# Kernel optimization log

Hardware: AMD Instinct MI355X
Metric: run time of the kernel (lower is better)

## Reference

```python
import jax, jax.numpy as jnp
import numpy as np

N_NODES = 100000
N_EDGES = 3200000
IN_CH = 128
HID = 64
OUT_CH = 2
BN_EPS = 1e-5


def setup_inputs() -> dict:
    key = jax.random.key(0)
    ks = jax.random.split(key, 16)
    def glorot(k, shape):
        fan_in, fan_out = shape[0], shape[1]
        lim = jnp.sqrt(6.0 / (fan_in + fan_out))
        return jax.random.uniform(k, shape, jnp.float32, -lim, lim)
    inp = {
        "x": jax.random.normal(ks[0], (N_NODES, IN_CH), jnp.float32),
        "edge_index": jax.random.randint(ks[1], (2, N_EDGES), 0, N_NODES, jnp.int64),
        # input projection + input BN
        "Wp": glorot(ks[2], (IN_CH, HID)),
        "bp": jnp.zeros((HID,), jnp.float32),
        "g_in": jnp.ones((HID,), jnp.float32),
        "b_in": jnp.zeros((HID,), jnp.float32),
        # SAGEConv layer 0: lin_l (aggr, with bias) + lin_r (self, no bias)
        "Wl0": glorot(ks[3], (HID, HID)),
        "bl0": jnp.zeros((HID,), jnp.float32),
        "Wr0": glorot(ks[4], (HID, HID)),
        "g0": jnp.ones((HID,), jnp.float32),
        "b0": jnp.zeros((HID,), jnp.float32),
        # SAGEConv layer 1
        "Wl1": glorot(ks[5], (HID, HID)),
        "bl1": jnp.zeros((HID,), jnp.float32),
        "Wr1": glorot(ks[6], (HID, HID)),
        "g1": jnp.ones((HID,), jnp.float32),
        "b1": jnp.zeros((HID,), jnp.float32),
        # output head
        "Wo": glorot(ks[7], (HID, OUT_CH)),
        "bo": jnp.zeros((OUT_CH,), jnp.float32),
    }
    return inp


def _bn(h, g, b):
    # training-mode batchnorm over node dim (biased variance, as torch)
    m = h.mean(axis=0)
    v = h.var(axis=0)
    return g * (h - m) * jax.lax.rsqrt(v + BN_EPS) + b


def _sage_conv(h, src, dst, Wl, bl, Wr):
    # mean aggregation of source features at destination nodes
    msg = h[src]                                              # [E, HID]
    summed = jax.ops.segment_sum(msg, dst, num_segments=N_NODES)
    cnt = jax.ops.segment_sum(jnp.ones((src.shape[0],), h.dtype), dst,
                              num_segments=N_NODES)
    aggr = summed / jnp.maximum(cnt, 1.0)[:, None]
    return aggr @ Wl + bl + h @ Wr


def reference(x, edge_index, Wp, bp, g_in, b_in,
              Wl0, bl0, Wr0, g0, b0,
              Wl1, bl1, Wr1, g1, b1,
              Wo, bo):
    src, dst = edge_index[0], edge_index[1]
    h = jax.nn.relu(_bn(x @ Wp + bp, g_in, b_in))   # dropout: eval no-op
    h_prev = h
    # layer 0 (i=0: no residual)
    h_new = jax.nn.relu(_bn(_sage_conv(h, src, dst, Wl0, bl0, Wr0), g0, b0))
    h_prev, h = h, h_new
    # layer 1 (i=1: residual with h_prev)
    h_new = jax.nn.relu(_bn(_sage_conv(h, src, dst, Wl1, bl1, Wr1), g1, b1))
    h_new = h_new + h_prev
    h = h_new
    return h @ Wo + bo
```

## Files before the change

### kernel.cpp

```cpp
#include <hip/hip_runtime.h>
#include <hip/hip_bf16.h>

#define NN 100000
#define NE 3200000
#define IC 128
#define HD 64
#define BN_EPS 1e-5f
#define NBUK 196
#define MSB 16

__device__ __forceinline__ float bf2f(unsigned short u) {
  return __uint_as_float(((unsigned)u) << 16);
}
__device__ __forceinline__ unsigned int f2bf(float f) {
  unsigned int u = __float_as_uint(f);
  return (u + 0x7FFFu + ((u >> 16) & 1u)) >> 16;
}
__device__ __forceinline__ unsigned int pack2(float a, float b) {
  return f2bf(a) | (f2bf(b) << 16);
}

__global__ __launch_bounds__(256) void k_gemm_in(
    const float* __restrict__ x, const float* __restrict__ Wp,
    const float* __restrict__ bp, unsigned int* __restrict__ pre16,
    float* __restrict__ stats) {
  __shared__ float sW[IC * HD];
  __shared__ unsigned int sXu[64 * 68];
  __shared__ float sStS[256], sStQ[256];
  int tid = threadIdx.x;
  for (int i = tid; i < IC * HD / 4; i += 256)
    *(float4*)&sW[i * 4] = *(const float4*)&Wp[i * 4];
  int cg = tid & 15, rg = tid >> 4;
  int c0 = cg * 4;
  float4 bpc = *(const float4*)&bp[c0];
  float S[4] = {0.f, 0.f, 0.f, 0.f}, Q[4] = {0.f, 0.f, 0.f, 0.f};
  const int NT = (NN + 63) / 64;
  for (int t = blockIdx.x; t < NT; t += gridDim.x) {
    int row0 = t * 64;
    __syncthreads();
    for (int i = tid; i < 1024; i += 256) {
      int r = i >> 4, k8 = i & 15;
      int grow = row0 + r;
      if (grow >= NN) grow = NN - 1;
      const float* xs = &x[(size_t)grow * IC + k8 * 8];
      float4 f0 = *(const float4*)xs;
      float4 f1 = *(const float4*)(xs + 4);
      uint4 p;
      p.x = pack2(f0.x, f0.y);
      p.y = pack2(f0.z, f0.w);
      p.z = pack2(f1.x, f1.y);
      p.w = pack2(f1.z, f1.w);
      *(uint4*)&sXu[r * 68 + k8 * 4] = p;
    }
    __syncthreads();
    float acc[4][4];
#pragma unroll
    for (int r = 0; r < 4; ++r)
#pragma unroll
      for (int c = 0; c < 4; ++c) acc[r][c] = ((const float*)&bpc)[c];
    for (int kg = 0; kg < IC; kg += 4) {
      uint2 xu[4];
      float4 wv[4];
#pragma unroll
      for (int r = 0; r < 4; ++r)
        xu[r] = *(const uint2*)&sXu[(rg * 4 + r) * 68 + (kg >> 1)];
#pragma unroll
      for (int j = 0; j < 4; ++j)
        wv[j] = *(const float4*)&sW[(kg + j) * HD + c0];
#pragma unroll
      for (int r = 0; r < 4; ++r) {
        float xv[4];
        xv[0] = __uint_as_float(xu[r].x << 16);
        xv[1] = __uint_as_float(xu[r].x & 0xFFFF0000u);
        xv[2] = __uint_as_float(xu[r].y << 16);
        xv[3] = __uint_as_float(xu[r].y & 0xFFFF0000u);
#pragma unroll
        for (int j = 0; j < 4; ++j) {
#pragma unroll
          for (int c = 0; c < 4; ++c)
            acc[r][c] = fmaf(xv[j], ((const float*)&wv[j])[c], acc[r][c]);
        }
      }
    }
#pragma unroll
    for (int r = 0; r < 4; ++r) {
      int row = row0 + rg * 4 + r;
      if (row < NN) {
        uint2 o;
        o.x = pack2(acc[r][0], acc[r][1]);
        o.y = pack2(acc[r][2], acc[r][3]);
        *(uint2*)&pre16[(size_t)row * 32 + cg * 2] = o;
#pragma unroll
        for (int c = 0; c < 4; ++c) {
          S[c] += acc[r][c];
          Q[c] = fmaf(acc[r][c], acc[r][c], Q[c]);
        }
      }
    }
  }
#pragma unroll
  for (int c = 0; c < 4; ++c) {
    S[c] += __shfl_xor(S[c], 16);
    S[c] += __shfl_xor(S[c], 32);
    Q[c] += __shfl_xor(Q[c], 16);
    Q[c] += __shfl_xor(Q[c], 32);
  }
  int wave = tid >> 6, lane = tid & 63;
  if (lane < 16) {
#pragma unroll
    for (int c = 0; c < 4; ++c) {
      sStS[wave * 64 + lane * 4 + c] = S[c];
      sStQ[wave * 64 + lane * 4 + c] = Q[c];
    }
  }
  __syncthreads();
  if (tid < 64) {
    float Ts = sStS[tid] + sStS[64 + tid] + sStS[128 + tid] + sStS[192 + tid];
    float Tq = sStQ[tid] + sStQ[64 + tid] + sStQ[128 + tid] + sStQ[192 + tid];
    atomicAdd(&stats[tid], Ts);
    atomicAdd(&stats[64 + tid], Tq);
  }
}

__global__ __launch_bounds__(256) void k_bn_relu(
    const unsigned int* __restrict__ pre16, const float* __restrict__ stats,
    const float* __restrict__ g, const float* __restrict__ b,
    unsigned int* __restrict__ h16u) {
  size_t i = (size_t)blockIdx.x * 256 + threadIdx.x;
  int c0 = ((int)(i & 15)) * 4;
  const float invN = 1.0f / NN;
  uint2 p = *(const uint2*)&pre16[i * 2];
  float v[4];
  v[0] = __uint_as_float(p.x << 16);
  v[1] = __uint_as_float(p.x & 0xFFFF0000u);
  v[2] = __uint_as_float(p.y << 16);
  v[3] = __uint_as_float(p.y & 0xFFFF0000u);
#pragma unroll
  for (int c = 0; c < 4; ++c) {
    float m = stats[c0 + c] * invN;
    float var = stats[64 + c0 + c] * invN - m * m;
    float sc = g[c0 + c] * rsqrtf(var + BN_EPS);
    v[c] = fmaxf((v[c] - m) * sc + b[c0 + c], 0.f);
  }
  uint2 o;
  o.x = pack2(v[0], v[1]);
  o.y = pack2(v[2], v[3]);
  *(uint2*)&h16u[i * 2] = o;
}

__global__ __launch_bounds__(256) void k_bhist(
    const int* __restrict__ dst, unsigned int* __restrict__ bcnt) {
  __shared__ unsigned int h[NBUK];
  for (int i = threadIdx.x; i < NBUK; i += 256) h[i] = 0u;
  __syncthreads();
  int i0 = blockIdx.x * 256 + threadIdx.x;
  int stride = gridDim.x * 256;
  for (int e = i0; e < NE; e += stride)
    atomicAdd(&h[((unsigned)dst[e]) >> 9], 1u);
  __syncthreads();
  for (int i = threadIdx.x; i < NBUK; i += 256)
    if (h[i]) atomicAdd(&bcnt[i], h[i]);
}

__global__ __launch_bounds__(256) void k_bscan(
    const unsigned int* __restrict__ bcnt, unsigned int* __restrict__ gstart,
    unsigned int* __restrict__ gcur) {
  __shared__ unsigned int s[256];
  int t = threadIdx.x;
  unsigned int my = (t < NBUK) ? bcnt[t] : 0u;
  s[t] = my;
  __syncthreads();
  for (int off = 1; off < 256; off <<= 1) {
    unsigned int v = (t >= off) ? s[t - off] : 0u;
    __syncthreads();
    s[t] += v;
    __syncthreads();
  }
  if (t < NBUK) {
    gstart[t] = s[t] - my;
    gcur[t] = s[t] - my;
  }
  if (t == NBUK - 1) gstart[NBUK] = s[t];
}

__global__ __launch_bounds__(256) void k_msplit(
    const int* __restrict__ src, const int* __restrict__ dst,
    unsigned int* __restrict__ gcur, unsigned int* __restrict__ staging) {
  __shared__ unsigned int hist[NBUK];
  __shared__ unsigned int gbase[NBUK];
  int tid = threadIdx.x;
  for (int i = tid; i < NBUK; i += 256) hist[i] = 0u;
  __syncthreads();
  int e0 = blockIdx.x * (256 * MSB);
  unsigned int pk[MSB], rk[MSB], bk[MSB];
#pragma unroll
  for (int i = 0; i < MSB; ++i) {
    int e = e0 + i * 256 + tid;
    if (e < NE) {
      int d = dst[e];
      unsigned int b = (unsigned int)(d >> 9);
      rk[i] = atomicAdd(&hist[b], 1u);
      pk[i] = (unsigned int)src[e] | ((unsigned int)(d & 511) << 17);
      bk[i] = b;
    } else {
      bk[i] = 0xFFFFFFFFu;
    }
  }
  __syncthreads();
  for (int i = tid; i < NBUK; i += 256)
    if (hist[i]) gbase[i] = atomicAdd(&gcur[i], hist[i]);
  __syncthreads();
#pragma unroll
  for (int i = 0; i < MSB; ++i)
    if (bk[i] != 0xFFFFFFFFu) staging[gbase[bk[i]] + rk[i]] = pk[i];
}

__global__ __launch_bounds__(512) void k_bucket_sort(
    const unsigned int* __restrict__ staging,
    const unsigned int* __restrict__ gstart, unsigned int* __restrict__ nstart,
    unsigned int* __restrict__ srcoff) {
  __shared__ unsigned int hist[512];
  __shared__ unsigned int sc[512];
  __shared__ unsigned int cur[512];
  int b = blockIdx.x, t = threadIdx.x;
  hist[t] = 0u;
  __syncthreads();
  int lo = (int)gstart[b], hi = (int)gstart[b + 1];
  for (int e = lo + t; e < hi; e += 512)
    atomicAdd(&hist[staging[e] >> 17], 1u);
  __syncthreads();
  unsigned int my = hist[t];
  sc[t] = my;
  __syncthreads();
  for (int off = 1; off < 512; off <<= 1) {
    unsigned int v = (t >= off) ? sc[t - off] : 0u;
    __syncthreads();
    sc[t] += v;
    __syncthreads();
  }
  unsigned int st = (unsigned int)lo + sc[t] - my;
  cur[t] = st;
  int node = b * 512 + t;
  if (node < NN) {
    nstart[node] = st;
    if (node == NN - 1) nstart[NN] = st + my;
  }
  __syncthreads();
  for (int e = lo + t; e < hi; e += 512) {
    unsigned int u = staging[e];
    unsigned int pos = atomicAdd(&cur[u >> 17], 1u);
    srcoff[pos] = (u & 0x1FFFFu) << 7;
  }
}

__global__ __launch_bounds__(256) void k_aggr_sorted(
    const unsigned int* __restrict__ srcoff,
    const unsigned int* __restrict__ nstart,
    const unsigned short* __restrict__ h16,
    unsigned short* __restrict__ a16) {
  int lane = threadIdx.x & 63;
  int n = (int)((blockIdx.x * 256 + threadIdx.x) >> 6);
  if (n >= NN) return;
  int g = lane >> 3;
  int q = lane & 7;
  int e0 = (int)nstart[n];
  int e1 = (int)nstart[n + 1];
  const char* hbase = (const char*)h16 + q * 16;
  float a0 = 0.f, a1 = 0.f, a2 = 0.f, a3 = 0.f;
  float a4 = 0.f, a5 = 0.f, a6 = 0.f, a7 = 0.f;
  float b0 = 0.f, b1 = 0.f, b2 = 0.f, b3 = 0.f;
  float b4 = 0.f, b5 = 0.f, b6 = 0.f, b7 = 0.f;
  int e = e0 + g;
  for (; e + 8 < e1; e += 16) {
    unsigned int o0 = srcoff[e];
    unsigned int o1 = srcoff[e + 8];
    uint4 u0 = *(const uint4*)(hbase + o0);
    uint4 u1 = *(const uint4*)(hbase + o1);
    a0 += __uint_as_float(u0.x << 16);
    a1 += __uint_as_float(u0.x & 0xFFFF0000u);
    a2 += __uint_as_float(u0.y << 16);
    a3 += __uint_as_float(u0.y & 0xFFFF0000u);
    a4 += __uint_as_float(u0.z << 16);
    a5 += __uint_as_float(u0.z & 0xFFFF0000u);
    a6 += __uint_as_float(u0.w << 16);
    a7 += __uint_as_float(u0.w & 0xFFFF0000u);
    b0 += __uint_as_float(u1.x << 16);
    b1 += __uint_as_float(u1.x & 0xFFFF0000u);
    b2 += __uint_as_float(u1.y << 16);
    b3 += __uint_as_float(u1.y & 0xFFFF0000u);
    b4 += __uint_as_float(u1.z << 16);
    b5 += __uint_as_float(u1.z & 0xFFFF0000u);
    b6 += __uint_as_float(u1.w << 16);
    b7 += __uint_as_float(u1.w & 0xFFFF0000u);
  }
  if (e < e1) {
    unsigned int o0 = srcoff[e];
    uint4 u0 = *(const uint4*)(hbase + o0);
    a0 += __uint_as_float(u0.x << 16);
    a1 += __uint_as_float(u0.x & 0xFFFF0000u);
    a2 += __uint_as_float(u0.y << 16);
    a3 += __uint_as_float(u0.y & 0xFFFF0000u);
    a4 += __uint_as_float(u0.z << 16);
    a5 += __uint_as_float(u0.z & 0xFFFF0000u);
    a6 += __uint_as_float(u0.w << 16);
    a7 += __uint_as_float(u0.w & 0xFFFF0000u);
  }
  a0 += b0; a1 += b1; a2 += b2; a3 += b3;
  a4 += b4; a5 += b5; a6 += b6; a7 += b7;
#pragma unroll
  for (int off = 8; off <= 32; off <<= 1) {
    a0 += __shfl_xor(a0, off);
    a1 += __shfl_xor(a1, off);
    a2 += __shfl_xor(a2, off);
    a3 += __shfl_xor(a3, off);
    a4 += __shfl_xor(a4, off);
    a5 += __shfl_xor(a5, off);
    a6 += __shfl_xor(a6, off);
    a7 += __shfl_xor(a7, off);
  }
  if (g == 0) {
    float cntf = (float)(e1 - e0);
    float inv = (cntf > 0.f) ? 1.0f / cntf : 0.f;
    uint4 o;
    o.x = pack2(a0 * inv, a1 * inv);
    o.y = pack2(a2 * inv, a3 * inv);
    o.z = pack2(a4 * inv, a5 * inv);
    o.w = pack2(a6 * inv, a7 * inv);
    *(uint4*)((char*)a16 + (size_t)n * 128 + q * 16) = o;
  }
}

__global__ __launch_bounds__(256) void k_combine(
    const unsigned int* __restrict__ a16u,
    const unsigned int* __restrict__ h16u, const float* __restrict__ Wl,
    const float* __restrict__ bl, const float* __restrict__ Wr,
    unsigned int* __restrict__ pre16, float* __restrict__ stats) {
  __shared__ float sWl[HD * HD], sWr[HD * HD];
  __shared__ unsigned int sAu[64 * 36], sHu[64 * 36];
  __shared__ float sStS[256], sStQ[256];
  int tid = threadIdx.x;
  for (int i = tid; i < HD * HD / 4; i += 256) {
    *(float4*)&sWl[i * 4] = *(const float4*)&Wl[i * 4];
    *(float4*)&sWr[i * 4] = *(const float4*)&Wr[i * 4];
  }
  int cg = tid & 15, rg = tid >> 4;
  int c0 = cg * 4;
  float4 blc = *(const float4*)&bl[c0];
  float S[4] = {0.f, 0.f, 0.f, 0.f}, Q[4] = {0.f, 0.f, 0.f, 0.f};
  const int NT = (NN + 63) / 64;
  for (int t = blockIdx.x; t < NT; t += gridDim.x) {
    int row0 = t * 64;
    __syncthreads();
    for (int i = tid; i < 512; i += 256) {
      int r = i >> 3, c4 = i & 7;
      int grow = row0 + r;
      if (grow >= NN) grow = NN - 1;
      *(uint4*)&sAu[r * 36 + c4 * 4] =
          *(const uint4*)&a16u[(size_t)grow * 32 + c4 * 4];
      *(uint4*)&sHu[r * 36 + c4 * 4] =
          *(const uint4*)&h16u[(size_t)grow * 32 + c4 * 4];
    }
    __syncthreads();
    float acc[4][4];
#pragma unroll
    for (int r = 0; r < 4; ++r)
#pragma unroll
      for (int c = 0; c < 4; ++c) acc[r][c] = ((const float*)&blc)[c];
    for (int kg = 0; kg < HD; kg += 4) {
      uint2 au[4], hu[4];
      float4 wlv[4], wrv[4];
#pragma unroll
      for (int r = 0; r < 4; ++r) {
        au[r] = *(const uint2*)&sAu[(rg * 4 + r) * 36 + (kg >> 1)];
        hu[r] = *(const uint2*)&sHu[(rg * 4 + r) * 36 + (kg >> 1)];
      }
#pragma unroll
      for (int j = 0; j < 4; ++j) {
        wlv[j] = *(const float4*)&sWl[(kg + j) * HD + c0];
        wrv[j] = *(const float4*)&sWr[(kg + j) * HD + c0];
      }
#pragma unroll
      for (int r = 0; r < 4; ++r) {
        float av[4], hv[4];
        av[0] = __uint_as_float(au[r].x << 16);
        av[1] = __uint_as_float(au[r].x & 0xFFFF0000u);
        av[2] = __uint_as_float(au[r].y << 16);
        av[3] = __uint_as_float(au[r].y & 0xFFFF0000u);
        hv[0] = __uint_as_float(hu[r].x << 16);
        hv[1] = __uint_as_float(hu[r].x & 0xFFFF0000u);
        hv[2] = __uint_as_float(hu[r].y << 16);
        hv[3] = __uint_as_float(hu[r].y & 0xFFFF0000u);
#pragma unroll
        for (int j = 0; j < 4; ++j) {
#pragma unroll
          for (int c = 0; c < 4; ++c) {
            acc[r][c] = fmaf(av[j], ((const float*)&wlv[j])[c], acc[r][c]);
            acc[r][c] = fmaf(hv[j], ((const float*)&wrv[j])[c], acc[r][c]);
          }
        }
      }
    }
#pragma unroll
    for (int r = 0; r < 4; ++r) {
      int row = row0 + rg * 4 + r;
      if (row < NN) {
        uint2 o;
        o.x = pack2(acc[r][0], acc[r][1]);
        o.y = pack2(acc[r][2], acc[r][3]);
        *(uint2*)&pre16[(size_t)row * 32 + cg * 2] = o;
#pragma unroll
        for (int c = 0; c < 4; ++c) {
          S[c] += acc[r][c];
          Q[c] = fmaf(acc[r][c], acc[r][c], Q[c]);
        }
      }
    }
  }
#pragma unroll
  for (int c = 0; c < 4; ++c) {
    S[c] += __shfl_xor(S[c], 16);
    S[c] += __shfl_xor(S[c], 32);
    Q[c] += __shfl_xor(Q[c], 16);
    Q[c] += __shfl_xor(Q[c], 32);
  }
  int wave = tid >> 6, lane = tid & 63;
  if (lane < 16) {
#pragma unroll
    for (int c = 0; c < 4; ++c) {
      sStS[wave * 64 + lane * 4 + c] = S[c];
      sStQ[wave * 64 + lane * 4 + c] = Q[c];
    }
  }
  __syncthreads();
  if (tid < 64) {
    float Ts = sStS[tid] + sStS[64 + tid] + sStS[128 + tid] + sStS[192 + tid];
    float Tq = sStQ[tid] + sStQ[64 + tid] + sStQ[128 + tid] + sStQ[192 + tid];
    atomicAdd(&stats[tid], Ts);
    atomicAdd(&stats[64 + tid], Tq);
  }
}

__global__ __launch_bounds__(256) void k_bn_relu_head(
    const unsigned short* __restrict__ pre16,
    const float* __restrict__ stats, const float* __restrict__ g,
    const float* __restrict__ b, const unsigned short* __restrict__ resid16,
    const float* __restrict__ Wo, const float* __restrict__ bo,
    float* __restrict__ out) {
  int lane = threadIdx.x & 63;
  int wid = (int)((blockIdx.x * blockDim.x + threadIdx.x) >> 6);
  int nw = (int)((gridDim.x * blockDim.x) >> 6);
  const float invN = 1.0f / NN;
  float m = stats[lane] * invN;
  float v = stats[64 + lane] * invN - m * m;
  float sc = g[lane] * rsqrtf(v + BN_EPS);
  float bb = b[lane];
  float w0 = Wo[lane * 2], w1 = Wo[lane * 2 + 1];
  float b0 = bo[0], b1 = bo[1];
  for (int row = wid; row < NN; row += nw) {
    size_t i = (size_t)row * HD + lane;
    float val = (bf2f(pre16[i]) - m) * sc + bb;
    val = fmaxf(val, 0.f) + bf2f(resid16[i]);
    float a0 = val * w0, a1 = val * w1;
#pragma unroll
    for (int off = 32; off > 0; off >>= 1) {
      a0 += __shfl_down(a0, off);
      a1 += __shfl_down(a1, off);
    }
    if (lane == 0) {
      out[(size_t)row * 2] = a0 + b0;
      out[(size_t)row * 2 + 1] = a1 + b1;
    }
  }
}

extern "C" void kernel_launch(void* const* d_in, const int* in_sizes, int n_in,
                              void* d_out, int out_size, void* d_ws,
                              size_t ws_size, hipStream_t stream) {
  const float* x = (const float*)d_in[0];
  const int* ei = (const int*)d_in[1];
  const float* Wp = (const float*)d_in[2];
  const float* bp = (const float*)d_in[3];
  const float* g_in = (const float*)d_in[4];
  const float* b_in = (const float*)d_in[5];
  const float* Wl0 = (const float*)d_in[6];
  const float* bl0 = (const float*)d_in[7];
  const float* Wr0 = (const float*)d_in[8];
  const float* g0 = (const float*)d_in[9];
  const float* b0 = (const float*)d_in[10];
  const float* Wl1 = (const float*)d_in[11];
  const float* bl1 = (const float*)d_in[12];
  const float* Wr1 = (const float*)d_in[13];
  const float* g1 = (const float*)d_in[14];
  const float* b1 = (const float*)d_in[15];
  const float* Wo = (const float*)d_in[16];
  const float* bo = (const float*)d_in[17];
  float* out = (float*)d_out;

  const int* src = ei;
  const int* dst = ei + NE;

  unsigned int* pre16 = (unsigned int*)d_ws;
  unsigned short* h0 = (unsigned short*)(pre16 + (size_t)NN * 32);
  unsigned short* h1 = h0 + (size_t)NN * HD;
  unsigned short* a16 = h1 + (size_t)NN * HD;
  unsigned int* staging = (unsigned int*)(a16 + (size_t)NN * HD);
  unsigned int* srcoff = staging + NE;
  unsigned int* nstart = srcoff + NE;
  unsigned int* bcnt = nstart + NN + 1;
  unsigned int* gstart = bcnt + NBUK;
  unsigned int* gcur = gstart + NBUK + 1;
  float* stats0 = (float*)(gcur + NBUK);
  float* stats1 = stats0 + 128;
  float* stats2 = stats1 + 128;

  const int BNR_BLOCKS = (NN * HD / 4) / 256;
  const int AGGR_BLOCKS = 25000;
  const int MS_BLOCKS = (NE + 256 * MSB - 1) / (256 * MSB);

  hipMemsetAsync(stats0, 0, 3 * 128 * sizeof(float), stream);
  hipMemsetAsync(bcnt, 0, NBUK * sizeof(unsigned int), stream);

  k_gemm_in<<<768, 256, 0, stream>>>(x, Wp, bp, pre16, stats0);
  k_bn_relu<<<BNR_BLOCKS, 256, 0, stream>>>(pre16, stats0, g_in, b_in,
                                            (unsigned int*)h0);

  k_bhist<<<1024, 256, 0, stream>>>(dst, bcnt);
  k_bscan<<<1, 256, 0, stream>>>(bcnt, gstart, gcur);
  k_msplit<<<MS_BLOCKS, 256, 0, stream>>>(src, dst, gcur, staging);
  k_bucket_sort<<<NBUK, 512, 0, stream>>>(staging, gstart, nstart, srcoff);

  k_aggr_sorted<<<AGGR_BLOCKS, 256, 0, stream>>>(srcoff, nstart, h0, a16);
  k_combine<<<768, 256, 0, stream>>>((const unsigned int*)a16,
                                     (const unsigned int*)h0, Wl0, bl0, Wr0,
                                     pre16, stats1);
  k_bn_relu<<<BNR_BLOCKS, 256, 0, stream>>>(pre16, stats1, g0, b0,
                                            (unsigned int*)h1);

  k_aggr_sorted<<<AGGR_BLOCKS, 256, 0, stream>>>(srcoff, nstart, h1, a16);
  k_combine<<<768, 256, 0, stream>>>((const unsigned int*)a16,
                                     (const unsigned int*)h1, Wl1, bl1, Wr1,
                                     pre16, stats2);
  k_bn_relu_head<<<1024, 256, 0, stream>>>((const unsigned short*)pre16,
                                           stats2, g1, b1, h0, Wo, bo, out);
}
```

Baseline: 395.8 us.

## Drop dst histogram pass via fixed-capacity buckets; one tile per GEMM block

```diff
diff --git a/kernel.cpp b/kernel.cpp
--- a/kernel.cpp
+++ b/kernel.cpp
@@ -8,6 +8,7 @@
 #define BN_EPS 1e-5f
 #define NBUK 196
 #define MSB 16
+#define CAP 20480
 
 __device__ __forceinline__ float bf2f(unsigned short u) {
   return __uint_as_float(((unsigned)u) << 16);
@@ -24,77 +25,70 @@
     const float* __restrict__ x, const float* __restrict__ Wp,
     const float* __restrict__ bp, unsigned int* __restrict__ pre16,
     float* __restrict__ stats) {
-  __shared__ float sW[IC * HD];
   __shared__ unsigned int sXu[64 * 68];
   __shared__ float sStS[256], sStQ[256];
   int tid = threadIdx.x;
-  for (int i = tid; i < IC * HD / 4; i += 256)
-    *(float4*)&sW[i * 4] = *(const float4*)&Wp[i * 4];
   int cg = tid & 15, rg = tid >> 4;
   int c0 = cg * 4;
+  int row0 = blockIdx.x * 64;
+  for (int i = tid; i < 1024; i += 256) {
+    int r = i >> 4, k8 = i & 15;
+    int grow = row0 + r;
+    if (grow >= NN) grow = NN - 1;
+    const float* xs = &x[(size_t)grow * IC + k8 * 8];
+    float4 f0 = *(const float4*)xs;
+    float4 f1 = *(const float4*)(xs + 4);
+    uint4 p;
+    p.x = pack2(f0.x, f0.y);
+    p.y = pack2(f0.z, f0.w);
+    p.z = pack2(f1.x, f1.y);
+    p.w = pack2(f1.z, f1.w);
+    *(uint4*)&sXu[r * 68 + k8 * 4] = p;
+  }
+  __syncthreads();
   float4 bpc = *(const float4*)&bp[c0];
+  float acc[4][4];
+#pragma unroll
+  for (int r = 0; r < 4; ++r)
+#pragma unroll
+    for (int c = 0; c < 4; ++c) acc[r][c] = ((const float*)&bpc)[c];
+  for (int kg = 0; kg < IC; kg += 4) {
+    uint2 xu[4];
+    float4 wv[4];
+#pragma unroll
+    for (int r = 0; r < 4; ++r)
+      xu[r] = *(const uint2*)&sXu[(rg * 4 + r) * 68 + (kg >> 1)];
+#pragma unroll
+    for (int j = 0; j < 4; ++j)
+      wv[j] = *(const float4*)&Wp[(size_t)(kg + j) * HD + c0];
+#pragma unroll
+    for (int r = 0; r < 4; ++r) {
+      float xv[4];
+      xv[0] = __uint_as_float(xu[r].x << 16);
+      xv[1] = __uint_as_float(xu[r].x & 0xFFFF0000u);
+      xv[2] = __uint_as_float(xu[r].y << 16);
+      xv[3] = __uint_as_float(xu[r].y & 0xFFFF0000u);
+#pragma unroll
+      for (int j = 0; j < 4; ++j) {
+#pragma unroll
+        for (int c = 0; c < 4; ++c)
+          acc[r][c] = fmaf(xv[j], ((const float*)&wv[j])[c], acc[r][c]);
+      }
+    }
+  }
   float S[4] = {0.f, 0.f, 0.f, 0.f}, Q[4] = {0.f, 0.f, 0.f, 0.f};
-  const int NT = (NN + 63) / 64;
-  for (int t = blockIdx.x; t < NT; t += gridDim.x) {
-    int row0 = t * 64;
-    __syncthreads();
-    for (int i = tid; i < 1024; i += 256) {
-      int r = i >> 4, k8 = i & 15;
-      int grow = row0 + r;
-      if (grow >= NN) grow = NN - 1;
-      const float* xs = &x[(size_t)grow * IC + k8 * 8];
-      float4 f0 = *(const float4*)xs;
-      float4 f1 = *(const float4*)(xs + 4);
-      uint4 p;
-      p.x = pack2(f0.x, f0.y);
-      p.y = pack2(f0.z, f0.w);
-      p.z = pack2(f1.x, f1.y);
-      p.w = pack2(f1.z, f1.w);
-      *(uint4*)&sXu[r * 68 + k8 * 4] = p;
-    }
-    __syncthreads();
-    float acc[4][4];
-#pragma unroll
-    for (int r = 0; r < 4; ++r)
-#pragma unroll
-      for (int c = 0; c < 4; ++c) acc[r][c] = ((const float*)&bpc)[c];
-    for (int kg = 0; kg < IC; kg += 4) {
-      uint2 xu[4];
-      float4 wv[4];
-#pragma unroll
-      for (int r = 0; r < 4; ++r)
-        xu[r] = *(const uint2*)&sXu[(rg * 4 + r) * 68 + (kg >> 1)];
-#pragma unroll
-      for (int j = 0; j < 4; ++j)
-        wv[j] = *(const float4*)&sW[(kg + j) * HD + c0];
-#pragma unroll
-      for (int r = 0; r < 4; ++r) {
-        float xv[4];
-        xv[0] = __uint_as_float(xu[r].x << 16);
-        xv[1] = __uint_as_float(xu[r].x & 0xFFFF0000u);
-        xv[2] = __uint_as_float(xu[r].y << 16);
-        xv[3] = __uint_as_float(xu[r].y & 0xFFFF0000u);
-#pragma unroll
-        for (int j = 0; j < 4; ++j) {
-#pragma unroll
-          for (int c = 0; c < 4; ++c)
-            acc[r][c] = fmaf(xv[j], ((const float*)&wv[j])[c], acc[r][c]);
-        }
-      }
-    }
-#pragma unroll
-    for (int r = 0; r < 4; ++r) {
-      int row = row0 + rg * 4 + r;
-      if (row < NN) {
-        uint2 o;
-        o.x = pack2(acc[r][0], acc[r][1]);
-        o.y = pack2(acc[r][2], acc[r][3]);
-        *(uint2*)&pre16[(size_t)row * 32 + cg * 2] = o;
-#pragma unroll
-        for (int c = 0; c < 4; ++c) {
-          S[c] += acc[r][c];
-          Q[c] = fmaf(acc[r][c], acc[r][c], Q[c]);
-        }
+#pragma unroll
+  for (int r = 0; r < 4; ++r) {
+    int row = row0 + rg * 4 + r;
+    if (row < NN) {
+      uint2 o;
+      o.x = pack2(acc[r][0], acc[r][1]);
+      o.y = pack2(acc[r][2], acc[r][3]);
+      *(uint2*)&pre16[(size_t)row * 32 + cg * 2] = o;
+#pragma unroll
+      for (int c = 0; c < 4; ++c) {
+        S[c] += acc[r][c];
+        Q[c] = fmaf(acc[r][c], acc[r][c], Q[c]);
       }
     }
   }
@@ -148,39 +142,9 @@
   *(uint2*)&h16u[i * 2] = o;
 }
 
-__global__ __launch_bounds__(256) void k_bhist(
-    const int* __restrict__ dst, unsigned int* __restrict__ bcnt) {
-  __shared__ unsigned int h[NBUK];
-  for (int i = threadIdx.x; i < NBUK; i += 256) h[i] = 0u;
-  __syncthreads();
-  int i0 = blockIdx.x * 256 + threadIdx.x;
-  int stride = gridDim.x * 256;
-  for (int e = i0; e < NE; e += stride)
-    atomicAdd(&h[((unsigned)dst[e]) >> 9], 1u);
-  __syncthreads();
-  for (int i = threadIdx.x; i < NBUK; i += 256)
-    if (h[i]) atomicAdd(&bcnt[i], h[i]);
-}
-
-__global__ __launch_bounds__(256) void k_bscan(
-    const unsigned int* __restrict__ bcnt, unsigned int* __restrict__ gstart,
-    unsigned int* __restrict__ gcur) {
-  __shared__ unsigned int s[256];
+__global__ __launch_bounds__(256) void k_initcur(unsigned int* __restrict__ gcur) {
   int t = threadIdx.x;
-  unsigned int my = (t < NBUK) ? bcnt[t] : 0u;
-  s[t] = my;
-  __syncthreads();
-  for (int off = 1; off < 256; off <<= 1) {
-    unsigned int v = (t >= off) ? s[t - off] : 0u;
-    __syncthreads();
-    s[t] += v;
-    __syncthreads();
-  }
-  if (t < NBUK) {
-    gstart[t] = s[t] - my;
-    gcur[t] = s[t] - my;
-  }
-  if (t == NBUK - 1) gstart[NBUK] = s[t];
+  if (t < NBUK) gcur[t] = (unsigned int)(t * CAP);
 }
 
 __global__ __launch_bounds__(256) void k_msplit(
@@ -215,6 +179,23 @@
     if (bk[i] != 0xFFFFFFFFu) staging[gbase[bk[i]] + rk[i]] = pk[i];
 }
 
+__global__ __launch_bounds__(256) void k_cscan(
+    const unsigned int* __restrict__ gcur, unsigned int* __restrict__ gstart) {
+  __shared__ unsigned int s[256];
+  int t = threadIdx.x;
+  unsigned int my = (t < NBUK) ? (gcur[t] - (unsigned int)(t * CAP)) : 0u;
+  s[t] = my;
+  __syncthreads();
+  for (int off = 1; off < 256; off <<= 1) {
+    unsigned int v = (t >= off) ? s[t - off] : 0u;
+    __syncthreads();
+    s[t] += v;
+    __syncthreads();
+  }
+  if (t < NBUK) gstart[t] = s[t] - my;
+  if (t == NBUK - 1) gstart[NBUK] = s[t];
+}
+
 __global__ __launch_bounds__(512) void k_bucket_sort(
     const unsigned int* __restrict__ staging,
     const unsigned int* __restrict__ gstart, unsigned int* __restrict__ nstart,
@@ -225,9 +206,11 @@
   int b = blockIdx.x, t = threadIdx.x;
   hist[t] = 0u;
   __syncthreads();
-  int lo = (int)gstart[b], hi = (int)gstart[b + 1];
-  for (int e = lo + t; e < hi; e += 512)
-    atomicAdd(&hist[staging[e] >> 17], 1u);
+  int base_in = b * CAP;
+  int lo = (int)gstart[b];
+  int cnt = (int)gstart[b + 1] - lo;
+  for (int i = t; i < cnt; i += 512)
+    atomicAdd(&hist[staging[base_in + i] >> 17], 1u);
   __syncthreads();
   unsigned int my = hist[t];
   sc[t] = my;
@@ -246,8 +229,8 @@
     if (node == NN - 1) nstart[NN] = st + my;
   }
   __syncthreads();
-  for (int e = lo + t; e < hi; e += 512) {
-    unsigned int u = staging[e];
+  for (int i = t; i < cnt; i += 512) {
+    unsigned int u = staging[base_in + i];
     unsigned int pos = atomicAdd(&cur[u >> 17], 1u);
     srcoff[pos] = (u & 0x1FFFFu) << 7;
   }
@@ -335,84 +318,75 @@
     const unsigned int* __restrict__ h16u, const float* __restrict__ Wl,
     const float* __restrict__ bl, const float* __restrict__ Wr,
     unsigned int* __restrict__ pre16, float* __restrict__ stats) {
-  __shared__ float sWl[HD * HD], sWr[HD * HD];
   __shared__ unsigned int sAu[64 * 36], sHu[64 * 36];
   __shared__ float sStS[256], sStQ[256];
   int tid = threadIdx.x;
-  for (int i = tid; i < HD * HD / 4; i += 256) {
-    *(float4*)&sWl[i * 4] = *(const float4*)&Wl[i * 4];
-    *(float4*)&sWr[i * 4] = *(const float4*)&Wr[i * 4];
-  }
   int cg = tid & 15, rg = tid >> 4;
   int c0 = cg * 4;
+  int row0 = blockIdx.x * 64;
+  for (int i = tid; i < 512; i += 256) {
+    int r = i >> 3, c4 = i & 7;
+    int grow = row0 + r;
+    if (grow >= NN) grow = NN - 1;
+    *(uint4*)&sAu[r * 36 + c4 * 4] =
+        *(const uint4*)&a16u[(size_t)grow * 32 + c4 * 4];
+    *(uint4*)&sHu[r * 36 + c4 * 4] =
+        *(const uint4*)&h16u[(size_t)grow * 32 + c4 * 4];
+  }
+  __syncthreads();
   float4 blc = *(const float4*)&bl[c0];
-  float S[4] = {0.f, 0.f, 0.f, 0.f}, Q[4] = {0.f, 0.f, 0.f, 0.f};
-  const int NT = (NN + 63) / 64;
-  for (int t = blockIdx.x; t < NT; t += gridDim.x) {
-    int row0 = t * 64;
-    __syncthreads();
-    for (int i = tid; i < 512; i += 256) {
-      int r = i >> 3, c4 = i & 7;
-      int grow = row0 + r;
-      if (grow >= NN) grow = NN - 1;
-      *(uint4*)&sAu[r * 36 + c4 * 4] =
-          *(const uint4*)&a16u[(size_t)grow * 32 + c4 * 4];
-      *(uint4*)&sHu[r * 36 + c4 * 4] =
-          *(const uint4*)&h16u[(size_t)grow * 32 + c4 * 4];
-    }
-    __syncthreads();
-    float acc[4][4];
-#pragma unroll
-    for (int r = 0; r < 4; ++r)
-#pragma unroll
-      for (int c = 0; c < 4; ++c) acc[r][c] = ((const float*)&blc)[c];
-    for (int kg = 0; kg < HD; kg += 4) {
-      uint2 au[4], hu[4];
-      float4 wlv[4], wrv[4];
-#pragma unroll
-      for (int r = 0; r < 4; ++r) {
-        au[r] = *(const uint2*)&sAu[(rg * 4 + r) * 36 + (kg >> 1)];
-        hu[r] = *(const uint2*)&sHu[(rg * 4 + r) * 36 + (kg >> 1)];
-      }
+  float acc[4][4];
+#pragma unroll
+  for (int r = 0; r < 4; ++r)
+#pragma unroll
+    for (int c = 0; c < 4; ++c) acc[r][c] = ((const float*)&blc)[c];
+  for (int kg = 0; kg < HD; kg += 4) {
+    uint2 au[4], hu[4];
+    float4 wlv[4], wrv[4];
+#pragma unroll
+    for (int r = 0; r < 4; ++r) {
+      au[r] = *(const uint2*)&sAu[(rg * 4 + r) * 36 + (kg >> 1)];
+      hu[r] = *(const uint2*)&sHu[(rg * 4 + r) * 36 + (kg >> 1)];
+    }
+#pragma unroll
+    for (int j = 0; j < 4; ++j) {
+      wlv[j] = *(const float4*)&Wl[(size_t)(kg + j) * HD + c0];
+      wrv[j] = *(const float4*)&Wr[(size_t)(kg + j) * HD + c0];
+    }
+#pragma unroll
+    for (int r = 0; r < 4; ++r) {
+      float av[4], hv[4];
+      av[0] = __uint_as_float(au[r].x << 16);
+      av[1] = __uint_as_float(au[r].x & 0xFFFF0000u);
+      av[2] = __uint_as_float(au[r].y << 16);
+      av[3] = __uint_as_float(au[r].y & 0xFFFF0000u);
+      hv[0] = __uint_as_float(hu[r].x << 16);
+      hv[1] = __uint_as_float(hu[r].x & 0xFFFF0000u);
+      hv[2] = __uint_as_float(hu[r].y << 16);
+      hv[3] = __uint_as_float(hu[r].y & 0xFFFF0000u);
 #pragma unroll
       for (int j = 0; j < 4; ++j) {
-        wlv[j] = *(const float4*)&sWl[(kg + j) * HD + c0];
-        wrv[j] = *(const float4*)&sWr[(kg + j) * HD + c0];
-      }
-#pragma unroll
-      for (int r = 0; r < 4; ++r) {
-        float av[4], hv[4];
-        av[0] = __uint_as_float(au[r].x << 16);
-        av[1] = __uint_as_float(au[r].x & 0xFFFF0000u);
-        av[2] = __uint_as_float(au[r].y << 16);
-        av[3] = __uint_as_float(au[r].y & 0xFFFF0000u);
-        hv[0] = __uint_as_float(hu[r].x << 16);
-        hv[1] = __uint_as_float(hu[r].x & 0xFFFF0000u);
-        hv[2] = __uint_as_float(hu[r].y << 16);
-        hv[3] = __uint_as_float(hu[r].y & 0xFFFF0000u);
-#pragma unroll
-        for (int j = 0; j < 4; ++j) {
-#pragma unroll
-          for (int c = 0; c < 4; ++c) {
-            acc[r][c] = fmaf(av[j], ((const float*)&wlv[j])[c], acc[r][c]);
-            acc[r][c] = fmaf(hv[j], ((const float*)&wrv[j])[c], acc[r][c]);
-          }
+#pragma unroll
+        for (int c = 0; c < 4; ++c) {
+          acc[r][c] = fmaf(av[j], ((const float*)&wlv[j])[c], acc[r][c]);
+          acc[r][c] = fmaf(hv[j], ((const float*)&wrv[j])[c], acc[r][c]);
         }
       }
     }
-#pragma unroll
-    for (int r = 0; r < 4; ++r) {
-      int row = row0 + rg * 4 + r;
-      if (row < NN) {
-        uint2 o;
-        o.x = pack2(acc[r][0], acc[r][1]);
-        o.y = pack2(acc[r][2], acc[r][3]);
-        *(uint2*)&pre16[(size_t)row * 32 + cg * 2] = o;
-#pragma unroll
-        for (int c = 0; c < 4; ++c) {
-          S[c] += acc[r][c];
-          Q[c] = fmaf(acc[r][c], acc[r][c], Q[c]);
-        }
+  }
+  float S[4] = {0.f, 0.f, 0.f, 0.f}, Q[4] = {0.f, 0.f, 0.f, 0.f};
+#pragma unroll
+  for (int r = 0; r < 4; ++r) {
+    int row = row0 + rg * 4 + r;
+    if (row < NN) {
+      uint2 o;
+      o.x = pack2(acc[r][0], acc[r][1]);
+      o.y = pack2(acc[r][2], acc[r][3]);
+      *(uint2*)&pre16[(size_t)row * 32 + cg * 2] = o;
+#pragma unroll
+      for (int c = 0; c < 4; ++c) {
+        S[c] += acc[r][c];
+        Q[c] = fmaf(acc[r][c], acc[r][c], Q[c]);
       }
     }
   }
@@ -504,10 +478,9 @@
   unsigned short* h1 = h0 + (size_t)NN * HD;
   unsigned short* a16 = h1 + (size_t)NN * HD;
   unsigned int* staging = (unsigned int*)(a16 + (size_t)NN * HD);
-  unsigned int* srcoff = staging + NE;
+  unsigned int* srcoff = staging + (size_t)NBUK * CAP;
   unsigned int* nstart = srcoff + NE;
-  unsigned int* bcnt = nstart + NN + 1;
-  unsigned int* gstart = bcnt + NBUK;
+  unsigned int* gstart = nstart + NN + 1;
   unsigned int* gcur = gstart + NBUK + 1;
   float* stats0 = (float*)(gcur + NBUK);
   float* stats1 = stats0 + 128;
@@ -516,30 +489,30 @@
   const int BNR_BLOCKS = (NN * HD / 4) / 256;
   const int AGGR_BLOCKS = 25000;
   const int MS_BLOCKS = (NE + 256 * MSB - 1) / (256 * MSB);
+  const int TILE_BLOCKS = (NN + 63) / 64;
 
   hipMemsetAsync(stats0, 0, 3 * 128 * sizeof(float), stream);
-  hipMemsetAsync(bcnt, 0, NBUK * sizeof(unsigned int), stream);
-
-  k_gemm_in<<<768, 256, 0, stream>>>(x, Wp, bp, pre16, stats0);
+
+  k_gemm_in<<<TILE_BLOCKS, 256, 0, stream>>>(x, Wp, bp, pre16, stats0);
   k_bn_relu<<<BNR_BLOCKS, 256, 0, stream>>>(pre16, stats0, g_in, b_in,
                                             (unsigned int*)h0);
 
-  k_bhist<<<1024, 256, 0, stream>>>(dst, bcnt);
-  k_bscan<<<1, 256, 0, stream>>>(bcnt, gstart, gcur);
+  k_initcur<<<1, 256, 0, stream>>>(gcur);
   k_msplit<<<MS_BLOCKS, 256, 0, stream>>>(src, dst, gcur, staging);
+  k_cscan<<<1, 256, 0, stream>>>(gcur, gstart);
   k_bucket_sort<<<NBUK, 512, 0, stream>>>(staging, gstart, nstart, srcoff);
 
   k_aggr_sorted<<<AGGR_BLOCKS, 256, 0, stream>>>(srcoff, nstart, h0, a16);
-  k_combine<<<768, 256, 0, stream>>>((const unsigned int*)a16,
-                                     (const unsigned int*)h0, Wl0, bl0, Wr0,
-                                     pre16, stats1);
+  k_combine<<<TILE_BLOCKS, 256, 0, stream>>>((const unsigned int*)a16,
+                                             (const unsigned int*)h0, Wl0,
+                                             bl0, Wr0, pre16, stats1);
   k_bn_relu<<<BNR_BLOCKS, 256, 0, stream>>>(pre16, stats1, g0, b0,
                                             (unsigned int*)h1);
 
   k_aggr_sorted<<<AGGR_BLOCKS, 256, 0, stream>>>(srcoff, nstart, h1, a16);
-  k_combine<<<768, 256, 0, stream>>>((const unsigned int*)a16,
-                                     (const unsigned int*)h1, Wl1, bl1, Wr1,
-                                     pre16, stats2);
+  k_combine<<<TILE_BLOCKS, 256, 0, stream>>>((const unsigned int*)a16,
+                                             (const unsigned int*)h1, Wl1,
+                                             bl1, Wr1, pre16, stats2);
   k_bn_relu_head<<<1024, 256, 0, stream>>>((const unsigned short*)pre16,
                                            stats2, g1, b1, h0, Wo, bo, out);
 }
```

Measured after the change: 463.8 us. 1.17x slower.
